# Optimization experiments

Measured on AMD Instinct MI355X. Metric: run time of the kernel, lower is better.

The kernel has to match this reference:

```python
import jax, jax.numpy as jnp
import numpy as np

N_WIDTH = 16
N_ORDER = 3
N_ELEMENTS = 64
N_NODES = N_ELEMENTS * N_ORDER + 1  # 193
N_SAMPLES = 4096
X_MIN = 0.0
X_MAX = 1.0
NDIM_IN = 2


def setup_inputs() -> dict:
    key = jax.random.key(0)
    k1, k2 = jax.random.split(key)
    x = jax.random.uniform(k1, (N_SAMPLES, NDIM_IN), dtype=jnp.float32)  # in [x_min, x_max]
    # torch init is zeros; use small random values so outputs/grads are informative
    weight = 0.1 * jax.random.normal(k2, (N_WIDTH, N_NODES, NDIM_IN), dtype=jnp.float32)
    return {"x": x, "weight": weight}


def _lagrange_all(xr, nodes):
    """phi, dphi, ddphi of the (n_order+1) Lagrange basis at xr (S,W,D).
    Returns three arrays of shape (S,W,P,D), P = n_order+1. Loops are over the
    tiny fixed basis size only; everything is vectorized over (S,W,D)."""
    P = len(nodes)
    phi, dphi, ddphi = [], [], []
    for j in range(P):
        # value
        p = jnp.ones_like(xr)
        for m in range(P):
            if m != j:
                p = p * (xr - nodes[m]) / (nodes[j] - nodes[m])
        phi.append(p)
        # first derivative
        y1 = jnp.zeros_like(xr)
        for i in range(P):
            if i == j:
                continue
            k = jnp.full_like(xr, 1.0 / (nodes[j] - nodes[i]))
            for m in range(P):
                if m != i and m != j:
                    k = k * (xr - nodes[m]) / (nodes[j] - nodes[m])
            y1 = y1 + k
        dphi.append(y1)
        # second derivative
        y2 = jnp.zeros_like(xr)
        for i in range(P):
            if i == j:
                continue
            ks = jnp.zeros_like(xr)
            for m in range(P):
                if m != i and m != j:
                    kp = jnp.full_like(xr, 1.0 / (nodes[j] - nodes[m]))
                    for n in range(P):
                        if n != i and n != j and n != m:
                            kp = kp * (xr - nodes[n]) / (nodes[j] - nodes[n])
                    ks = ks + kp
            y2 = y2 + ks / (nodes[j] - nodes[i])
        ddphi.append(y2)
    return jnp.stack(phi, 2), jnp.stack(dphi, 2), jnp.stack(ddphi, 2)


def _forward(x, weight):
    S, W, D, P = N_SAMPLES, N_WIDTH, NDIM_IN, N_ORDER + 1
    xw = jnp.broadcast_to(x[:, None, :], (S, W, D))  # (S,W,D)
    x_shift = (N_NODES - 1) * (xw - X_MIN) / (X_MAX - X_MIN)
    id_el = jnp.clip(jnp.floor(x_shift / N_ORDER), 0, N_ELEMENTS - 1)
    nodes_l = (id_el * N_ORDER).astype(jnp.int32)  # (S,W,D), left node index
    # nodes_r - nodes_l == n_order
    x_ref = 2.0 * (x_shift - nodes_l) / N_ORDER - 1.0
    delta_x = 0.5 * N_ORDER * (X_MAX - X_MIN) / (N_NODES - 1)

    nodes = [float(v) for v in np.linspace(-1.0, 1.0, P)]
    phi_l, dphi_l, ddphi_l = _lagrange_all(x_ref, nodes)  # (S,W,P,D)
    dphi_l = dphi_l / delta_x
    ddphi_l = ddphi_l / (delta_x * delta_x)

    # Scatter local basis values into global node axis (vectorized replacement
    # of the quadruple Python loop in the original).
    ii = jnp.arange(S)[:, None, None, None]
    kk = jnp.arange(W)[None, :, None, None]
    dd = jnp.arange(D)[None, None, None, :]
    pp = nodes_l[:, :, None, :] + jnp.arange(P)[None, None, :, None]  # (S,W,P,D)
    zeros = jnp.zeros((S, W, N_NODES, D), dtype=x.dtype)
    phi = zeros.at[ii, kk, pp, dd].set(phi_l)
    dphi = zeros.at[ii, kk, pp, dd].set(dphi_l)
    ddphi = zeros.at[ii, kk, pp, dd].set(ddphi_l)

    t_ik = jnp.einsum('kpj,ikpj->ik', weight, phi)
    dt_ik = jnp.einsum('kpj,ikpj->ik', weight, dphi)
    ddt_ik = jnp.einsum('kpj,ikpj->ik', weight, ddphi)
    return t_ik, dt_ik, ddt_ik, phi, dphi, ddphi, delta_x


def reference(x, weight):
    # returns (t_ik, dt_ik, ddt_ik, phi_ikpj, dphi_ikpj, ddphi_ikpj, delta_x)
    return _forward(x, weight)
```

## Files before the change

### kernel.cpp

```cpp
#include <hip/hip_runtime.h>

typedef float f32x4 __attribute__((ext_vector_type(4)));

constexpr int S  = 4096;
constexpr int W  = 16;
constexpr int NN = 193;
constexpr int DD = 2;
constexpr int SW = S * W;
constexpr int PHI_OFF = 3 * SW;
constexpr int PHI_SZ  = SW * NN * DD;
constexpr long DX_OFF = (long)PHI_OFF + 3L * PHI_SZ;

constexpr int ROW_F    = NN * DD;
constexpr int CHUNK_F4 = W * ROW_F / 4;

__device__ __forceinline__ void basis(int a, float xvd, int& nl,
                                      float& c0, float& c1, float& c2, float& c3) {
    float xs = 192.0f * xvd;
    float fe = floorf(xs * (1.0f / 3.0f));
    fe = fminf(fmaxf(fe, 0.0f), 63.0f);
    nl = (int)(fe * 3.0f);
    float xr = 2.0f * (xs - (float)nl) * (1.0f / 3.0f) - 1.0f;

    const float k0 = 0.5625f;
    const float k1 = 1.6875f;
    float xp1 = xr + 1.0f;
    float xm1 = xr - 1.0f;
    float x2  = xr * xr;
    float x2m = x2 - (1.0f / 9.0f);

    if (a == 0) {
        c0 = -k0 * x2m * xm1;
        c1 =  k1 * xp1 * (xr - (1.0f / 3.0f)) * xm1;
        c2 = -k1 * xp1 * (xr + (1.0f / 3.0f)) * xm1;
        c3 =  k0 * xp1 * x2m;
    } else if (a == 1) {
        const float s1 = 128.0f;
        c0 = -k0 * (3.0f * x2 - 2.0f * xr - (1.0f / 9.0f)) * s1;
        c1 =  k1 * (3.0f * x2 - (2.0f / 3.0f) * xr - 1.0f) * s1;
        c2 = -k1 * (3.0f * x2 + (2.0f / 3.0f) * xr - 1.0f) * s1;
        c3 =  k0 * (3.0f * x2 + 2.0f * xr - (1.0f / 9.0f)) * s1;
    } else {
        const float s2 = 16384.0f;
        c0 = -k0 * (6.0f * xr - 2.0f) * s2;
        c1 =  k1 * (6.0f * xr - (2.0f / 3.0f)) * s2;
        c2 = -k1 * (6.0f * xr + (2.0f / 3.0f)) * s2;
        c3 =  k0 * (6.0f * xr + 2.0f) * s2;
    }
}

__device__ __forceinline__ float pick4(int rel, float c0, float c1, float c2, float c3) {
    float r = 0.0f;
    r = (rel == 0) ? c0 : r;
    r = (rel == 1) ? c1 : r;
    r = (rel == 2) ? c2 : r;
    r = (rel == 3) ? c3 : r;
    return r;
}

__global__ __launch_bounds__(256)
void kan_kernel(const float* __restrict__ x,
                const float* __restrict__ w,
                float* __restrict__ out) {
    const int b   = blockIdx.x;
    const int a   = b >> 12;
    const int i   = b & 4095;
    const int tid = threadIdx.x;

    const float xv0 = x[2 * i];
    const float xv1 = x[2 * i + 1];

    int nl0, nl1;
    float v00, v01, v02, v03, v10, v11, v12, v13;
    basis(a, xv0, nl0, v00, v01, v02, v03);
    basis(a, xv1, nl1, v10, v11, v12, v13);

    if (tid < W) {
        const float* wk = w + tid * ROW_F;
        float s = 0.0f;
        s += wk[(nl0 + 0) * 2 + 0] * v00;
        s += wk[(nl0 + 1) * 2 + 0] * v01;
        s += wk[(nl0 + 2) * 2 + 0] * v02;
        s += wk[(nl0 + 3) * 2 + 0] * v03;
        s += wk[(nl1 + 0) * 2 + 1] * v10;
        s += wk[(nl1 + 1) * 2 + 1] * v11;
        s += wk[(nl1 + 2) * 2 + 1] * v12;
        s += wk[(nl1 + 3) * 2 + 1] * v13;
        out[a * SW + i * W + tid] = s;
    }
    if (b == 0 && tid == 0)
        out[DX_OFF] = 0.0078125f;

    f32x4* dst = (f32x4*)(out + PHI_OFF + (size_t)a * PHI_SZ)
                 + (size_t)i * CHUNK_F4;

    int e = 4 * tid;
    if (e >= 772) e -= 772;
    else if (e >= 386) e -= 386;

    for (int p = tid; p < CHUNK_F4; p += 256) {
        f32x4 vv;
#pragma unroll
        for (int j = 0; j < 4; ++j) {
            int ee = e + j;
            if (ee >= ROW_F) ee -= ROW_F;
            int n = ee >> 1;
            float p0 = pick4(n - nl0, v00, v01, v02, v03);
            float p1 = pick4(n - nl1, v10, v11, v12, v13);
            vv[j] = (ee & 1) ? p1 : p0;
        }
        dst[p] = vv;
        e += (256 * 4) % ROW_F;
        if (e >= ROW_F) e -= ROW_F;
    }
}

extern "C" void kernel_launch(void* const* d_in, const int* in_sizes, int n_in,
                              void* d_out, int out_size, void* d_ws, size_t ws_size,
                              hipStream_t stream) {
    const float* x = (const float*)d_in[0];
    const float* w = (const float*)d_in[1];
    float* out = (float*)d_out;

    kan_kernel<<<3 * S, 256, 0, stream>>>(x, w, out);
}
```

Before: 303.1 us.

## Zero-fill basis outputs with memset and scatter only nonzero entries

Replaces the per-element dense generation of the phi/dphi/ddphi tensors with a hipMemsetAsync zero fill plus a small kernel that writes only the four nonzero local basis values per (sample, width, dim, derivative). One block per sample now computes all three derivative orders and the weighted sums. This removes the costly per-element select logic from the bandwidth-heavy write path. The trade-off is an extra launch, and scattered scalar stores that land on lines the memset already wrote.

```diff
diff --git a/kernel.cpp b/kernel.cpp
--- a/kernel.cpp
+++ b/kernel.cpp
@@ -1,6 +1,4 @@
 #include <hip/hip_runtime.h>
-
-typedef float f32x4 __attribute__((ext_vector_type(4)));
 
 constexpr int S  = 4096;
 constexpr int W  = 16;
@@ -10,12 +8,9 @@
 constexpr int PHI_OFF = 3 * SW;
 constexpr int PHI_SZ  = SW * NN * DD;
 constexpr long DX_OFF = (long)PHI_OFF + 3L * PHI_SZ;
+constexpr int ROW_F = NN * DD;
 
-constexpr int ROW_F    = NN * DD;
-constexpr int CHUNK_F4 = W * ROW_F / 4;
-
-__device__ __forceinline__ void basis(int a, float xvd, int& nl,
-                                      float& c0, float& c1, float& c2, float& c3) {
+__device__ __forceinline__ void basis_a(int a, float xvd, int& nl, float c[4]) {
     float xs = 192.0f * xvd;
     float fe = floorf(xs * (1.0f / 3.0f));
     fe = fminf(fmaxf(fe, 0.0f), 63.0f);
@@ -24,95 +19,70 @@
 
     const float k0 = 0.5625f;
     const float k1 = 1.6875f;
+    float x2  = xr * xr;
+    float x2m = x2 - (1.0f / 9.0f);
     float xp1 = xr + 1.0f;
     float xm1 = xr - 1.0f;
-    float x2  = xr * xr;
-    float x2m = x2 - (1.0f / 9.0f);
 
     if (a == 0) {
-        c0 = -k0 * x2m * xm1;
-        c1 =  k1 * xp1 * (xr - (1.0f / 3.0f)) * xm1;
-        c2 = -k1 * xp1 * (xr + (1.0f / 3.0f)) * xm1;
-        c3 =  k0 * xp1 * x2m;
+        c[0] = -k0 * x2m * xm1;
+        c[1] =  k1 * xp1 * (xr - (1.0f / 3.0f)) * xm1;
+        c[2] = -k1 * xp1 * (xr + (1.0f / 3.0f)) * xm1;
+        c[3] =  k0 * xp1 * x2m;
     } else if (a == 1) {
         const float s1 = 128.0f;
-        c0 = -k0 * (3.0f * x2 - 2.0f * xr - (1.0f / 9.0f)) * s1;
-        c1 =  k1 * (3.0f * x2 - (2.0f / 3.0f) * xr - 1.0f) * s1;
-        c2 = -k1 * (3.0f * x2 + (2.0f / 3.0f) * xr - 1.0f) * s1;
-        c3 =  k0 * (3.0f * x2 + 2.0f * xr - (1.0f / 9.0f)) * s1;
+        c[0] = -k0 * (3.0f * x2 - 2.0f * xr - (1.0f / 9.0f)) * s1;
+        c[1] =  k1 * (3.0f * x2 - (2.0f / 3.0f) * xr - 1.0f) * s1;
+        c[2] = -k1 * (3.0f * x2 + (2.0f / 3.0f) * xr - 1.0f) * s1;
+        c[3] =  k0 * (3.0f * x2 + 2.0f * xr - (1.0f / 9.0f)) * s1;
     } else {
         const float s2 = 16384.0f;
-        c0 = -k0 * (6.0f * xr - 2.0f) * s2;
-        c1 =  k1 * (6.0f * xr - (2.0f / 3.0f)) * s2;
-        c2 = -k1 * (6.0f * xr + (2.0f / 3.0f)) * s2;
-        c3 =  k0 * (6.0f * xr + 2.0f) * s2;
+        c[0] = -k0 * (6.0f * xr - 2.0f) * s2;
+        c[1] =  k1 * (6.0f * xr - (2.0f / 3.0f)) * s2;
+        c[2] = -k1 * (6.0f * xr + (2.0f / 3.0f)) * s2;
+        c[3] =  k0 * (6.0f * xr + 2.0f) * s2;
     }
 }
 
-__device__ __forceinline__ float pick4(int rel, float c0, float c1, float c2, float c3) {
-    float r = 0.0f;
-    r = (rel == 0) ? c0 : r;
-    r = (rel == 1) ? c1 : r;
-    r = (rel == 2) ? c2 : r;
-    r = (rel == 3) ? c3 : r;
-    return r;
-}
-
-__global__ __launch_bounds__(256)
-void kan_kernel(const float* __restrict__ x,
-                const float* __restrict__ w,
-                float* __restrict__ out) {
-    const int b   = blockIdx.x;
-    const int a   = b >> 12;
-    const int i   = b & 4095;
+__global__ __launch_bounds__(384)
+void kan_scatter(const float* __restrict__ x,
+                 const float* __restrict__ w,
+                 float* __restrict__ out) {
+    const int i   = blockIdx.x;
     const int tid = threadIdx.x;
 
-    const float xv0 = x[2 * i];
-    const float xv1 = x[2 * i + 1];
+    {
+        int a = tid >> 7;
+        int r = tid & 127;
+        int k = r >> 3;
+        int d = (r >> 2) & 1;
+        int p = r & 3;
+        float xv = x[2 * i + d];
+        int nl; float c[4];
+        basis_a(a, xv, nl, c);
+        float v = (p == 0) ? c[0] : (p == 1) ? c[1] : (p == 2) ? c[2] : c[3];
+        out[(size_t)PHI_OFF + (size_t)a * PHI_SZ
+            + (size_t)i * (W * ROW_F) + k * ROW_F + (nl + p) * 2 + d] = v;
+    }
 
-    int nl0, nl1;
-    float v00, v01, v02, v03, v10, v11, v12, v13;
-    basis(a, xv0, nl0, v00, v01, v02, v03);
-    basis(a, xv1, nl1, v10, v11, v12, v13);
+    if (tid < 48) {
+        int a2 = tid % 3;
+        int kk = tid / 3;
+        int nl0, nl1; float c0[4], c1[4];
+        basis_a(a2, x[2 * i],     nl0, c0);
+        basis_a(a2, x[2 * i + 1], nl1, c1);
+        const float* wk = w + kk * ROW_F;
+        float s = 0.0f;
+#pragma unroll
+        for (int p = 0; p < 4; ++p) {
+            s += wk[(nl0 + p) * 2 + 0] * c0[p];
+            s += wk[(nl1 + p) * 2 + 1] * c1[p];
+        }
+        out[a2 * SW + i * W + kk] = s;
+    }
 
-    if (tid < W) {
-        const float* wk = w + tid * ROW_F;
-        float s = 0.0f;
-        s += wk[(nl0 + 0) * 2 + 0] * v00;
-        s += wk[(nl0 + 1) * 2 + 0] * v01;
-        s += wk[(nl0 + 2) * 2 + 0] * v02;
-        s += wk[(nl0 + 3) * 2 + 0] * v03;
-        s += wk[(nl1 + 0) * 2 + 1] * v10;
-        s += wk[(nl1 + 1) * 2 + 1] * v11;
-        s += wk[(nl1 + 2) * 2 + 1] * v12;
-        s += wk[(nl1 + 3) * 2 + 1] * v13;
-        out[a * SW + i * W + tid] = s;
-    }
-    if (b == 0 && tid == 0)
+    if (i == 0 && tid == 0)
         out[DX_OFF] = 0.0078125f;
-
-    f32x4* dst = (f32x4*)(out + PHI_OFF + (size_t)a * PHI_SZ)
-                 + (size_t)i * CHUNK_F4;
-
-    int e = 4 * tid;
-    if (e >= 772) e -= 772;
-    else if (e >= 386) e -= 386;
-
-    for (int p = tid; p < CHUNK_F4; p += 256) {
-        f32x4 vv;
-#pragma unroll
-        for (int j = 0; j < 4; ++j) {
-            int ee = e + j;
-            if (ee >= ROW_F) ee -= ROW_F;
-            int n = ee >> 1;
-            float p0 = pick4(n - nl0, v00, v01, v02, v03);
-            float p1 = pick4(n - nl1, v10, v11, v12, v13);
-            vv[j] = (ee & 1) ? p1 : p0;
-        }
-        dst[p] = vv;
-        e += (256 * 4) % ROW_F;
-        if (e >= ROW_F) e -= ROW_F;
-    }
 }
 
 extern "C" void kernel_launch(void* const* d_in, const int* in_sizes, int n_in,
@@ -122,5 +92,7 @@
     const float* w = (const float*)d_in[1];
     float* out = (float*)d_out;
 
-    kan_kernel<<<3 * S, 256, 0, stream>>>(x, w, out);
+    hipMemsetAsync(out + PHI_OFF, 0, 3L * PHI_SZ * sizeof(float), stream);
+
+    kan_scatter<<<S, 384, 0, stream>>>(x, w, out);
 }
```

Measured after the change: 336.3 us. 1.11x slower.
